# Performance work log

Measured on AMD Instinct MI355X. Metric: run time of the kernel, lower is better.

The kernel has to match this reference:

```python
import jax, jax.numpy as jnp
import numpy as np

B, S, E, H = 4, 2048, 1024, 8
D = E // H  # head_dim = 128


def setup_inputs() -> dict:
    key = jax.random.key(0)
    ks = jax.random.split(key, 7)
    scale = 1.0 / np.sqrt(D)
    return {
        "sequences": jax.random.normal(ks[0], (B, S, E), dtype=jnp.float32),
        # per-head Linear weights, torch layout [out, in] stacked over heads
        "Wq": jax.random.normal(ks[1], (H, D, D), dtype=jnp.float32) * scale,
        "Wk": jax.random.normal(ks[2], (H, D, D), dtype=jnp.float32) * scale,
        "Wv": jax.random.normal(ks[3], (H, D, D), dtype=jnp.float32) * scale,
        "bq": jax.random.normal(ks[4], (H, D), dtype=jnp.float32) * scale,
        "bk": jax.random.normal(ks[5], (H, D), dtype=jnp.float32) * scale,
        "bv": jax.random.normal(ks[6], (H, D), dtype=jnp.float32) * scale,
    }


def reference(sequences, Wq, Wk, Wv, bq, bk, bv):
    # split feature dim into heads: [B,S,H,D]
    xh = sequences.reshape(B, S, H, D)
    # torch Linear: y = x @ W.T + b  ->  contract input dim d with W[h, o, d]
    q = jnp.einsum("bshd,hod->bsho", xh, Wq) + bq
    k = jnp.einsum("bshd,hod->bsho", xh, Wk) + bk
    v = jnp.einsum("bshd,hod->bsho", xh, Wv) + bv
    # NOTE: original scales by 1/sqrt(num_heads), not 1/sqrt(head_dim)
    scores = jnp.einsum("bshd,bthd->bhst", q, k) / jnp.sqrt(jnp.float32(H))
    attn = jax.nn.softmax(scores, axis=-1)  # [B,H,S,S]
    out = jnp.einsum("bhst,bthd->bshd", attn, v)
    # hstack over heads == reshape back to [B,S,E]
    return out.reshape(B, S, E)
```

## Files before the change

### kernel.cpp

```cpp
#include <hip/hip_runtime.h>
#include <hip/hip_bf16.h>

#define B_ 4
#define S_ 2048
#define E_ 1024
#define H_ 8
#define D_ 128

using f16x8 = __attribute__((ext_vector_type(8))) _Float16;
using f32x4 = __attribute__((ext_vector_type(4))) float;

__device__ __forceinline__ ushort f2h_bits(float f) {
    union { _Float16 h; ushort u; } cv; cv.h = (_Float16)f; return cv.u;
}
__device__ __forceinline__ f16x8 pack8(const float* __restrict__ p) {
    float4 f0 = *(const float4*)p;
    float4 f1 = *(const float4*)(p + 4);
    f16x8 r;
    r[0] = (_Float16)f0.x; r[1] = (_Float16)f0.y;
    r[2] = (_Float16)f0.z; r[3] = (_Float16)f0.w;
    r[4] = (_Float16)f1.x; r[5] = (_Float16)f1.y;
    r[6] = (_Float16)f1.z; r[7] = (_Float16)f1.w;
    return r;
}

__device__ __forceinline__ void gll16(const ushort* g, ushort* l) {
    __builtin_amdgcn_global_load_lds(
        (const __attribute__((address_space(1))) unsigned int*)g,
        (__attribute__((address_space(3))) unsigned int*)l, 16, 0, 0);
}

__global__ __launch_bounds__(256) void kv_proj(
    const float* __restrict__ seq,
    const float* __restrict__ Wk, const float* __restrict__ Wv,
    const float* __restrict__ bk, const float* __restrict__ bv,
    ushort* __restrict__ ko, ushort* __restrict__ vo)
{
    constexpr int TS = 136;
    __shared__ ushort Tk[128 * TS];
    __shared__ ushort Tv[128 * TS];
    const int m0 = blockIdx.x * 128, h = blockIdx.y;
    const int tid = threadIdx.x, lane = tid & 63, w = tid >> 6;
    const int l16 = lane & 15, quad = lane >> 4;

    f16x8 a[2][4];
    #pragma unroll
    for (int mt = 0; mt < 2; ++mt)
        #pragma unroll
        for (int ks = 0; ks < 4; ++ks)
            a[mt][ks] = pack8(&seq[(size_t)(m0 + w * 32 + mt * 16 + l16) * E_
                                   + h * D_ + ks * 32 + quad * 8]);

    {
        const float* W = Wk + (size_t)h * D_ * D_;
        f32x4 acc[2][8];
        #pragma unroll
        for (int mt = 0; mt < 2; ++mt)
            #pragma unroll
            for (int nt = 0; nt < 8; ++nt) { f32x4 z = {0.f,0.f,0.f,0.f}; acc[mt][nt] = z; }
        #pragma unroll
        for (int ks = 0; ks < 4; ++ks)
            #pragma unroll
            for (int nt = 0; nt < 8; ++nt) {
                f16x8 bfr = pack8(&W[(size_t)(nt * 16 + l16) * D_ + ks * 32 + quad * 8]);
                #pragma unroll
                for (int mt = 0; mt < 2; ++mt)
                    acc[mt][nt] = __builtin_amdgcn_mfma_f32_16x16x32_f16(
                        a[mt][ks], bfr, acc[mt][nt], 0, 0, 0);
            }
        #pragma unroll
        for (int nt = 0; nt < 8; ++nt) {
            int o = nt * 16 + l16;
            float bias = bk[h * D_ + o];
            #pragma unroll
            for (int mt = 0; mt < 2; ++mt)
                #pragma unroll
                for (int r = 0; r < 4; ++r) {
                    int row = w * 32 + mt * 16 + quad * 4 + r;
                    Tk[row * TS + (o ^ (quad << 3))] = f2h_bits(acc[mt][nt][r] + bias);
                }
        }
    }
    {
        const float* W = Wv + (size_t)h * D_ * D_;
        f32x4 acc[2][8];
        #pragma unroll
        for (int mt = 0; mt < 2; ++mt)
            #pragma unroll
            for (int nt = 0; nt < 8; ++nt) { f32x4 z = {0.f,0.f,0.f,0.f}; acc[mt][nt] = z; }
        #pragma unroll
        for (int ks = 0; ks < 4; ++ks)
            #pragma unroll
            for (int nt = 0; nt < 8; ++nt) {
                f16x8 bfr = pack8(&W[(size_t)(nt * 16 + l16) * D_ + ks * 32 + quad * 8]);
                #pragma unroll
                for (int mt = 0; mt < 2; ++mt)
                    acc[mt][nt] = __builtin_amdgcn_mfma_f32_16x16x32_f16(
                        a[mt][ks], bfr, acc[mt][nt], 0, 0, 0);
            }
        #pragma unroll
        for (int nt = 0; nt < 8; ++nt) {
            int o = nt * 16 + l16;
            float bias = bv[h * D_ + o];
            #pragma unroll
            for (int mt = 0; mt < 2; ++mt)
                #pragma unroll
                for (int r = 0; r < 4; ++r) {
                    int row = w * 32 + mt * 16 + quad * 4 + r;
                    Tv[o * TS + row] = f2h_bits(acc[mt][nt][r] + bias);
                }
        }
    }
    __syncthreads();

    #pragma unroll
    for (int i = 0; i < 8; ++i) {
        int idx = tid + i * 256;
        int row = idx >> 4, c8 = (idx & 15) * 8;
        int lk = c8 ^ ((row & 7) << 3);
        uint4 dk = *(uint4*)&Tk[row * TS + (lk ^ (((row >> 2) & 3) << 3))];
        int m = m0 + row, bi = m >> 11, s = m & (S_ - 1);
        *(uint4*)&ko[(((size_t)bi * H_ + h) * S_ + s) * D_ + c8] = dk;
        uint4 dv = *(uint4*)&Tv[row * TS + (c8 ^ ((row & 7) << 3))];
        int mg = m0 + c8, bv_i = mg >> 11, s0 = mg & (S_ - 1);
        *(uint4*)&vo[(((size_t)bv_i * H_ + h) * D_ + row) * S_ + s0] = dv;
    }
}

__global__ __launch_bounds__(512) void attn(
    const float* __restrict__ seq, const float* __restrict__ Wq,
    const float* __restrict__ bq,
    const ushort* __restrict__ kg, const ushort* __restrict__ vtg,
    float* __restrict__ out)
{
    __shared__ alignas(16) ushort Kbuf[2][128 * 128];
    __shared__ alignas(16) ushort Vbuf[2][128 * 128];
    __shared__ alignas(16) ushort Pbuf[128 * 128];

    const int m0 = blockIdx.x * 128;
    const int h = blockIdx.y, bi = blockIdx.z;
    const int bh = bi * H_ + h;
    const int tid = threadIdx.x, lane = tid & 63, w = tid >> 6;
    const int l16 = lane & 15, quad = lane >> 4;
    const ushort* kbase = kg + (size_t)bh * S_ * D_;
    const ushort* vbase = vtg + (size_t)bh * D_ * S_;
    const float qscale = 0.35355339059327373f * 1.4426950408889634f;

    #pragma unroll
    for (int i = 0; i < 4; ++i) {
        int b = i * 8 + w;
        gll16(kbase + (size_t)b * 512 + lane * 8, &Kbuf[0][0] + b * 512);
        gll16(vbase + (size_t)(b * 4 + (lane >> 4)) * S_ + (lane & 15) * 8,
              &Vbuf[0][0] + b * 512);
    }

    {
        f16x8 xa[4];
        #pragma unroll
        for (int ks = 0; ks < 4; ++ks)
            xa[ks] = pack8(&seq[((size_t)bi * S_ + m0 + w * 16 + l16) * E_
                                + h * D_ + ks * 32 + quad * 8]);
        f32x4 qacc[8];
        #pragma unroll
        for (int nt = 0; nt < 8; ++nt) { f32x4 z = {0.f,0.f,0.f,0.f}; qacc[nt] = z; }
        const float* W = Wq + (size_t)h * D_ * D_;
        #pragma unroll
        for (int ks = 0; ks < 4; ++ks)
            #pragma unroll
            for (int nt = 0; nt < 8; ++nt) {
                f16x8 bfr = pack8(&W[(size_t)(nt * 16 + l16) * D_ + ks * 32 + quad * 8]);
                qacc[nt] = __builtin_amdgcn_mfma_f32_16x16x32_f16(
                    xa[ks], bfr, qacc[nt], 0, 0, 0);
            }
        #pragma unroll
        for (int nt = 0; nt < 8; ++nt) {
            int o = nt * 16 + l16;
            float bias = bq[h * D_ + o];
            #pragma unroll
            for (int r = 0; r < 4; ++r) {
                int row = w * 16 + quad * 4 + r;
                Pbuf[row * 128 + (o ^ (quad << 3))] =
                    f2h_bits((qacc[nt][r] + bias) * qscale);
            }
        }
    }
    f16x8 qf[4];
    #pragma unroll
    for (int ks = 0; ks < 4; ++ks)
        qf[ks] = *(const f16x8*)&Pbuf[(w * 16 + l16) * 128
                                      + ks * 32 + ((quad ^ (l16 >> 2)) << 3)];

    f32x4 o_acc[8];
    #pragma unroll
    for (int nt = 0; nt < 8; ++nt) { f32x4 z = {0.f,0.f,0.f,0.f}; o_acc[nt] = z; }
    float m_prev = -1e30f, l_lane = 0.f;

    __syncthreads();

    const int psw = (l16 & 7) << 1;
    const int kvsw = l16 & 7;

    for (int j = 0; j < S_ / 128; ++j) {
        const int cur = j & 1;
        const ushort* KL = &Kbuf[cur][0];
        const ushort* VL = &Vbuf[cur][0];

        if (j + 1 < S_ / 128) {
            const int n1 = (j + 1) * 128;
            const ushort* kt = kbase + (size_t)n1 * D_;
            const ushort* vt = vbase + n1;
            ushort* kd = &Kbuf[cur ^ 1][0];
            ushort* vd = &Vbuf[cur ^ 1][0];
            #pragma unroll
            for (int i = 0; i < 4; ++i) {
                int b = i * 8 + w;
                gll16(kt + (size_t)b * 512 + lane * 8, kd + b * 512);
                gll16(vt + (size_t)(b * 4 + (lane >> 4)) * S_ + (lane & 15) * 8,
                      vd + b * 512);
            }
        }

        f32x4 sacc[8];
        #pragma unroll
        for (int nt = 0; nt < 8; ++nt) { f32x4 z = {0.f,0.f,0.f,0.f}; sacc[nt] = z; }
        __builtin_amdgcn_s_setprio(1);
        #pragma unroll
        for (int ks = 0; ks < 4; ++ks)
            #pragma unroll
            for (int nt = 0; nt < 8; ++nt) {
                f16x8 kf = *(const f16x8*)&KL[(nt * 16 + l16) * 128
                                              + (((ks * 4 + quad) ^ kvsw) << 3)];
                sacc[nt] = __builtin_amdgcn_mfma_f32_16x16x32_f16(
                    kf, qf[ks], sacc[nt], 0, 0, 0);
            }
        __builtin_amdgcn_s_setprio(0);

        uint2 pkw[8];
        {
            float mx = fmaxf(fmaxf(sacc[0][0], sacc[0][1]), fmaxf(sacc[0][2], sacc[0][3]));
            #pragma unroll
            for (int nt = 1; nt < 8; ++nt)
                mx = fmaxf(mx, fmaxf(fmaxf(sacc[nt][0], sacc[nt][1]),
                                     fmaxf(sacc[nt][2], sacc[nt][3])));
            mx = fmaxf(mx, __shfl_xor(mx, 16));
            mx = fmaxf(mx, __shfl_xor(mx, 32));
            if (__any(mx > m_prev + 8.0f)) {
                float mnew  = fmaxf(m_prev, mx);
                float alpha = exp2f(m_prev - mnew);
                #pragma unroll
                for (int nt = 0; nt < 8; ++nt)
                    #pragma unroll
                    for (int r = 0; r < 4; ++r) o_acc[nt][r] *= alpha;
                l_lane *= alpha;
                m_prev = mnew;
            }
            #pragma unroll
            for (int nt = 0; nt < 8; ++nt) {
                float e0 = exp2f(sacc[nt][0] - m_prev);
                float e1 = exp2f(sacc[nt][1] - m_prev);
                float e2 = exp2f(sacc[nt][2] - m_prev);
                float e3 = exp2f(sacc[nt][3] - m_prev);
                auto p01 = __builtin_amdgcn_cvt_pkrtz(e0, e1);
                auto p23 = __builtin_amdgcn_cvt_pkrtz(e2, e3);
                l_lane += (float)p01[0] + (float)p01[1] + (float)p23[0] + (float)p23[1];
                pkw[nt] = make_uint2(__builtin_bit_cast(uint, p01),
                                     __builtin_bit_cast(uint, p23));
            }
        }

        const int qrow = w * 16 + l16;
        ushort* prow = &Pbuf[qrow * 128];
        #pragma unroll
        for (int nt = 0; nt < 8; ++nt)
            *(uint2*)&prow[((nt * 4 + quad) ^ psw) << 2] = pkw[nt];

        __builtin_amdgcn_s_setprio(1);
        #pragma unroll
        for (int ks = 0; ks < 4; ++ks) {
            f16x8 pb = *(const f16x8*)&prow[((ks * 8 + quad * 2) ^ psw) << 2];
            #pragma unroll
            for (int nt = 0; nt < 8; ++nt) {
                f16x8 vf = *(const f16x8*)&VL[(nt * 16 + l16) * 128
                                              + (((ks * 4 + quad) ^ kvsw) << 3)];
                o_acc[nt] = __builtin_amdgcn_mfma_f32_16x16x32_f16(
                    vf, pb, o_acc[nt], 0, 0, 0);
            }
        }
        __builtin_amdgcn_s_setprio(0);

        __syncthreads();
    }

    {
        float l = l_lane;
        l += __shfl_xor(l, 16);
        l += __shfl_xor(l, 32);
        float rinv = 1.0f / l;
        const int q = m0 + w * 16 + l16;
        #pragma unroll
        for (int nt = 0; nt < 8; ++nt) {
            float4 o;
            o.x = o_acc[nt][0] * rinv;
            o.y = o_acc[nt][1] * rinv;
            o.z = o_acc[nt][2] * rinv;
            o.w = o_acc[nt][3] * rinv;
            *(float4*)&out[((size_t)bi * S_ + q) * E_ + h * D_ + nt * 16 + quad * 4] = o;
        }
    }
}

extern "C" void kernel_launch(void* const* d_in, const int* in_sizes, int n_in,
                              void* d_out, int out_size, void* d_ws, size_t ws_size,
                              hipStream_t stream) {
    const float* seq = (const float*)d_in[0];
    const float* Wq  = (const float*)d_in[1];
    const float* Wk  = (const float*)d_in[2];
    const float* Wv  = (const float*)d_in[3];
    const float* bq  = (const float*)d_in[4];
    const float* bk  = (const float*)d_in[5];
    const float* bv  = (const float*)d_in[6];

    const size_t per = (size_t)B_ * H_ * S_ * D_;
    if (ws_size < 2 * per * sizeof(ushort)) return;
    ushort* kws  = (ushort*)d_ws;
    ushort* vtws = kws + per;

    kv_proj<<<dim3(B_ * S_ / 128, H_), 256, 0, stream>>>(
        seq, Wk, Wv, bk, bv, kws, vtws);
    attn<<<dim3(S_ / 128, H_, B_), 512, 0, stream>>>(
        seq, Wq, bq, kws, vtws, (float*)d_out);
}
```

Baseline: 279.6 us.

## Shrink KV tiles to 64 keys and reuse LDS to cut shared memory

The attention kernel now streams K/V in 64-key tiles instead of 128, halving the double-buffered K, V and P shared buffers. The Q staging area moves into the K buffer, so the first K load is issued only after Q fragments are read. The KV projection kernel processes 64 rows per block and reuses one LDS scratch buffer for K and V in turn. The aim is lower LDS use so more blocks can be resident per CU, at the cost of twice as many loop iterations, barriers and softmax rescale checks.

```diff
diff --git a/kernel.cpp b/kernel.cpp
--- a/kernel.cpp
+++ b/kernel.cpp
@@ -36,94 +36,84 @@
     const float* __restrict__ bk, const float* __restrict__ bv,
     ushort* __restrict__ ko, ushort* __restrict__ vo)
 {
-    constexpr int TS = 136;
-    __shared__ ushort Tk[128 * TS];
-    __shared__ ushort Tv[128 * TS];
-    const int m0 = blockIdx.x * 128, h = blockIdx.y;
+    __shared__ ushort T[128 * 68];
+    const int m0 = blockIdx.x * 64, h = blockIdx.y;
     const int tid = threadIdx.x, lane = tid & 63, w = tid >> 6;
     const int l16 = lane & 15, quad = lane >> 4;
 
-    f16x8 a[2][4];
-    #pragma unroll
-    for (int mt = 0; mt < 2; ++mt)
-        #pragma unroll
-        for (int ks = 0; ks < 4; ++ks)
-            a[mt][ks] = pack8(&seq[(size_t)(m0 + w * 32 + mt * 16 + l16) * E_
-                                   + h * D_ + ks * 32 + quad * 8]);
+    f16x8 a[4];
+    #pragma unroll
+    for (int ks = 0; ks < 4; ++ks)
+        a[ks] = pack8(&seq[(size_t)(m0 + w * 16 + l16) * E_
+                           + h * D_ + ks * 32 + quad * 8]);
 
     {
         const float* W = Wk + (size_t)h * D_ * D_;
-        f32x4 acc[2][8];
-        #pragma unroll
-        for (int mt = 0; mt < 2; ++mt)
-            #pragma unroll
-            for (int nt = 0; nt < 8; ++nt) { f32x4 z = {0.f,0.f,0.f,0.f}; acc[mt][nt] = z; }
+        f32x4 acc[8];
+        #pragma unroll
+        for (int nt = 0; nt < 8; ++nt) { f32x4 z = {0.f,0.f,0.f,0.f}; acc[nt] = z; }
         #pragma unroll
         for (int ks = 0; ks < 4; ++ks)
             #pragma unroll
             for (int nt = 0; nt < 8; ++nt) {
                 f16x8 bfr = pack8(&W[(size_t)(nt * 16 + l16) * D_ + ks * 32 + quad * 8]);
-                #pragma unroll
-                for (int mt = 0; mt < 2; ++mt)
-                    acc[mt][nt] = __builtin_amdgcn_mfma_f32_16x16x32_f16(
-                        a[mt][ks], bfr, acc[mt][nt], 0, 0, 0);
+                acc[nt] = __builtin_amdgcn_mfma_f32_16x16x32_f16(
+                    a[ks], bfr, acc[nt], 0, 0, 0);
             }
         #pragma unroll
         for (int nt = 0; nt < 8; ++nt) {
             int o = nt * 16 + l16;
             float bias = bk[h * D_ + o];
             #pragma unroll
-            for (int mt = 0; mt < 2; ++mt)
-                #pragma unroll
-                for (int r = 0; r < 4; ++r) {
-                    int row = w * 32 + mt * 16 + quad * 4 + r;
-                    Tk[row * TS + (o ^ (quad << 3))] = f2h_bits(acc[mt][nt][r] + bias);
-                }
-        }
-    }
+            for (int r = 0; r < 4; ++r) {
+                int row = w * 16 + quad * 4 + r;
+                T[row * 136 + (o ^ (quad << 3))] = f2h_bits(acc[nt][r] + bias);
+            }
+        }
+    }
+    __syncthreads();
+    #pragma unroll
+    for (int i = 0; i < 4; ++i) {
+        int idx = tid + i * 256;
+        int row = idx >> 4, c8 = (idx & 15) * 8;
+        int lk = c8 ^ ((row & 7) << 3);
+        uint4 dk = *(uint4*)&T[row * 136 + (lk ^ (((row >> 2) & 3) << 3))];
+        int m = m0 + row, bi = m >> 11, s = m & (S_ - 1);
+        *(uint4*)&ko[(((size_t)bi * H_ + h) * S_ + s) * D_ + c8] = dk;
+    }
+    __syncthreads();
     {
         const float* W = Wv + (size_t)h * D_ * D_;
-        f32x4 acc[2][8];
-        #pragma unroll
-        for (int mt = 0; mt < 2; ++mt)
-            #pragma unroll
-            for (int nt = 0; nt < 8; ++nt) { f32x4 z = {0.f,0.f,0.f,0.f}; acc[mt][nt] = z; }
+        f32x4 acc[8];
+        #pragma unroll
+        for (int nt = 0; nt < 8; ++nt) { f32x4 z = {0.f,0.f,0.f,0.f}; acc[nt] = z; }
         #pragma unroll
         for (int ks = 0; ks < 4; ++ks)
             #pragma unroll
             for (int nt = 0; nt < 8; ++nt) {
                 f16x8 bfr = pack8(&W[(size_t)(nt * 16 + l16) * D_ + ks * 32 + quad * 8]);
-                #pragma unroll
-                for (int mt = 0; mt < 2; ++mt)
-                    acc[mt][nt] = __builtin_amdgcn_mfma_f32_16x16x32_f16(
-                        a[mt][ks], bfr, acc[mt][nt], 0, 0, 0);
+                acc[nt] = __builtin_amdgcn_mfma_f32_16x16x32_f16(
+                    a[ks], bfr, acc[nt], 0, 0, 0);
             }
         #pragma unroll
         for (int nt = 0; nt < 8; ++nt) {
             int o = nt * 16 + l16;
             float bias = bv[h * D_ + o];
             #pragma unroll
-            for (int mt = 0; mt < 2; ++mt)
-                #pragma unroll
-                for (int r = 0; r < 4; ++r) {
-                    int row = w * 32 + mt * 16 + quad * 4 + r;
-                    Tv[o * TS + row] = f2h_bits(acc[mt][nt][r] + bias);
-                }
-        }
-    }
-    __syncthreads();
-
-    #pragma unroll
-    for (int i = 0; i < 8; ++i) {
+            for (int r = 0; r < 4; ++r) {
+                int row = w * 16 + quad * 4 + r;
+                T[o * 68 + row] = f2h_bits(acc[nt][r] + bias);
+            }
+        }
+    }
+    __syncthreads();
+    #pragma unroll
+    for (int i = 0; i < 4; ++i) {
         int idx = tid + i * 256;
-        int row = idx >> 4, c8 = (idx & 15) * 8;
-        int lk = c8 ^ ((row & 7) << 3);
-        uint4 dk = *(uint4*)&Tk[row * TS + (lk ^ (((row >> 2) & 3) << 3))];
-        int m = m0 + row, bi = m >> 11, s = m & (S_ - 1);
-        *(uint4*)&ko[(((size_t)bi * H_ + h) * S_ + s) * D_ + c8] = dk;
-        uint4 dv = *(uint4*)&Tv[row * TS + (c8 ^ ((row & 7) << 3))];
-        int mg = m0 + c8, bv_i = mg >> 11, s0 = mg & (S_ - 1);
-        *(uint4*)&vo[(((size_t)bv_i * H_ + h) * D_ + row) * S_ + s0] = dv;
+        int d = idx >> 3, c = idx & 7;
+        uint4 dv = *(uint4*)&T[d * 68 + ((c ^ (d & 7)) << 3)];
+        int bi = m0 >> 11, s0 = (m0 & (S_ - 1)) + c * 8;
+        *(uint4*)&vo[(((size_t)bi * H_ + h) * D_ + d) * S_ + s0] = dv;
     }
 }
 
@@ -133,27 +123,29 @@
     const ushort* __restrict__ kg, const ushort* __restrict__ vtg,
     float* __restrict__ out)
 {
-    __shared__ alignas(16) ushort Kbuf[2][128 * 128];
-    __shared__ alignas(16) ushort Vbuf[2][128 * 128];
-    __shared__ alignas(16) ushort Pbuf[128 * 128];
+    constexpr int NT = S_ / 64;
+    __shared__ alignas(16) ushort Kbuf[2][64 * 128];
+    __shared__ alignas(16) ushort Vbuf[2][128 * 64];
+    __shared__ alignas(16) ushort Pbuf[128 * 64];
 
     const int m0 = blockIdx.x * 128;
     const int h = blockIdx.y, bi = blockIdx.z;
     const int bh = bi * H_ + h;
     const int tid = threadIdx.x, lane = tid & 63, w = tid >> 6;
     const int l16 = lane & 15, quad = lane >> 4;
+    const int swz = l16 & 7;
     const ushort* kbase = kg + (size_t)bh * S_ * D_;
     const ushort* vbase = vtg + (size_t)bh * D_ * S_;
     const float qscale = 0.35355339059327373f * 1.4426950408889634f;
 
     #pragma unroll
-    for (int i = 0; i < 4; ++i) {
-        int b = i * 8 + w;
-        gll16(kbase + (size_t)b * 512 + lane * 8, &Kbuf[0][0] + b * 512);
-        gll16(vbase + (size_t)(b * 4 + (lane >> 4)) * S_ + (lane & 15) * 8,
-              &Vbuf[0][0] + b * 512);
-    }
-
+    for (int c = 0; c < 2; ++c) {
+        int i = w * 2 + c;
+        gll16(vbase + (size_t)(i * 8 + (lane >> 3)) * S_ + (lane & 7) * 8,
+              &Vbuf[0][0] + i * 512);
+    }
+
+    ushort* const Qs = &Kbuf[0][0];
     {
         f16x8 xa[4];
         #pragma unroll
@@ -179,16 +171,25 @@
             #pragma unroll
             for (int r = 0; r < 4; ++r) {
                 int row = w * 16 + quad * 4 + r;
-                Pbuf[row * 128 + (o ^ (quad << 3))] =
+                Qs[row * 128 + (o ^ (quad << 3))] =
                     f2h_bits((qacc[nt][r] + bias) * qscale);
             }
         }
     }
+    __syncthreads();
+
     f16x8 qf[4];
     #pragma unroll
     for (int ks = 0; ks < 4; ++ks)
-        qf[ks] = *(const f16x8*)&Pbuf[(w * 16 + l16) * 128
-                                      + ks * 32 + ((quad ^ (l16 >> 2)) << 3)];
+        qf[ks] = *(const f16x8*)&Qs[(w * 16 + l16) * 128
+                                    + ks * 32 + ((quad ^ (l16 >> 2)) << 3)];
+    __syncthreads();
+
+    #pragma unroll
+    for (int c = 0; c < 2; ++c) {
+        int i = w * 2 + c;
+        gll16(kbase + i * 512 + lane * 8, &Kbuf[0][0] + i * 512);
+    }
 
     f32x4 o_acc[8];
     #pragma unroll
@@ -197,49 +198,47 @@
 
     __syncthreads();
 
-    const int psw = (l16 & 7) << 1;
-    const int kvsw = l16 & 7;
-
-    for (int j = 0; j < S_ / 128; ++j) {
+    ushort* const prow = &Pbuf[(w * 16 + l16) * 64];
+
+    for (int j = 0; j < NT; ++j) {
         const int cur = j & 1;
         const ushort* KL = &Kbuf[cur][0];
         const ushort* VL = &Vbuf[cur][0];
 
-        if (j + 1 < S_ / 128) {
-            const int n1 = (j + 1) * 128;
-            const ushort* kt = kbase + (size_t)n1 * D_;
-            const ushort* vt = vbase + n1;
+        if (j + 1 < NT) {
+            const ushort* kt = kbase + (size_t)(j + 1) * 64 * 128;
+            const ushort* vt = vbase + (j + 1) * 64;
             ushort* kd = &Kbuf[cur ^ 1][0];
             ushort* vd = &Vbuf[cur ^ 1][0];
             #pragma unroll
-            for (int i = 0; i < 4; ++i) {
-                int b = i * 8 + w;
-                gll16(kt + (size_t)b * 512 + lane * 8, kd + b * 512);
-                gll16(vt + (size_t)(b * 4 + (lane >> 4)) * S_ + (lane & 15) * 8,
-                      vd + b * 512);
-            }
-        }
-
-        f32x4 sacc[8];
-        #pragma unroll
-        for (int nt = 0; nt < 8; ++nt) { f32x4 z = {0.f,0.f,0.f,0.f}; sacc[nt] = z; }
+            for (int c = 0; c < 2; ++c) {
+                int i = w * 2 + c;
+                gll16(kt + i * 512 + lane * 8, kd + i * 512);
+                gll16(vt + (size_t)(i * 8 + (lane >> 3)) * S_ + (lane & 7) * 8,
+                      vd + i * 512);
+            }
+        }
+
+        f32x4 sacc[4];
+        #pragma unroll
+        for (int nt = 0; nt < 4; ++nt) { f32x4 z = {0.f,0.f,0.f,0.f}; sacc[nt] = z; }
         __builtin_amdgcn_s_setprio(1);
         #pragma unroll
         for (int ks = 0; ks < 4; ++ks)
             #pragma unroll
-            for (int nt = 0; nt < 8; ++nt) {
+            for (int nt = 0; nt < 4; ++nt) {
                 f16x8 kf = *(const f16x8*)&KL[(nt * 16 + l16) * 128
-                                              + (((ks * 4 + quad) ^ kvsw) << 3)];
+                                              + (((ks * 4 + quad) ^ swz) << 3)];
                 sacc[nt] = __builtin_amdgcn_mfma_f32_16x16x32_f16(
                     kf, qf[ks], sacc[nt], 0, 0, 0);
             }
         __builtin_amdgcn_s_setprio(0);
 
-        uint2 pkw[8];
+        uint2 pkw[4];
         {
             float mx = fmaxf(fmaxf(sacc[0][0], sacc[0][1]), fmaxf(sacc[0][2], sacc[0][3]));
             #pragma unroll
-            for (int nt = 1; nt < 8; ++nt)
+            for (int nt = 1; nt < 4; ++nt)
                 mx = fmaxf(mx, fmaxf(fmaxf(sacc[nt][0], sacc[nt][1]),
                                      fmaxf(sacc[nt][2], sacc[nt][3])));
             mx = fmaxf(mx, __shfl_xor(mx, 16));
@@ -255,7 +254,7 @@
                 m_prev = mnew;
             }
             #pragma unroll
-            for (int nt = 0; nt < 8; ++nt) {
+            for (int nt = 0; nt < 4; ++nt) {
                 float e0 = exp2f(sacc[nt][0] - m_prev);
                 float e1 = exp2f(sacc[nt][1] - m_prev);
                 float e2 = exp2f(sacc[nt][2] - m_prev);
@@ -268,20 +267,20 @@
             }
         }
 
-        const int qrow = w * 16 + l16;
-        ushort* prow = &Pbuf[qrow * 128];
-        #pragma unroll
-        for (int nt = 0; nt < 8; ++nt)
-            *(uint2*)&prow[((nt * 4 + quad) ^ psw) << 2] = pkw[nt];
+        #pragma unroll
+        for (int nt = 0; nt < 4; ++nt) {
+            int G = 2 * nt + (quad >> 1);
+            *(uint2*)&prow[((G ^ swz) << 3) + ((quad & 1) << 2)] = pkw[nt];
+        }
 
         __builtin_amdgcn_s_setprio(1);
         #pragma unroll
-        for (int ks = 0; ks < 4; ++ks) {
-            f16x8 pb = *(const f16x8*)&prow[((ks * 8 + quad * 2) ^ psw) << 2];
+        for (int ks = 0; ks < 2; ++ks) {
+            f16x8 pb = *(const f16x8*)&prow[((ks * 4 + quad) ^ swz) << 3];
             #pragma unroll
             for (int nt = 0; nt < 8; ++nt) {
-                f16x8 vf = *(const f16x8*)&VL[(nt * 16 + l16) * 128
-                                              + (((ks * 4 + quad) ^ kvsw) << 3)];
+                f16x8 vf = *(const f16x8*)&VL[(nt * 16 + l16) * 64
+                                              + (((ks * 4 + quad) ^ swz) << 3)];
                 o_acc[nt] = __builtin_amdgcn_mfma_f32_16x16x32_f16(
                     vf, pb, o_acc[nt], 0, 0, 0);
             }
@@ -325,7 +324,7 @@
     ushort* kws  = (ushort*)d_ws;
     ushort* vtws = kws + per;
 
-    kv_proj<<<dim3(B_ * S_ / 128, H_), 256, 0, stream>>>(
+    kv_proj<<<dim3(B_ * S_ / 64, H_), 256, 0, stream>>>(
         seq, Wk, Wv, bk, bv, kws, vtws);
     attn<<<dim3(S_ / 128, H_, B_), 512, 0, stream>>>(
         seq, Wq, bq, kws, vtws, (float*)d_out);
```

After: 280.0 us. Within noise of the previous version (+0.2%).
